# Kernel optimization log

Hardware: AMD Instinct MI355X
Metric: run time of the kernel (lower is better)

The kernel has to match this reference:

```python
import jax, jax.numpy as jnp
import numpy as np

NH = 4
MAX_BUF = 1024
EPS = 1e-5


def _ln(x, w, b):
    mu = jnp.mean(x, axis=-1, keepdims=True)
    var = jnp.var(x, axis=-1, keepdims=True)
    return (x - mu) * jax.lax.rsqrt(var + EPS) * w + b


def _mha(xq, xkv, w_qkv, b_qkv, w_o, b_o, key_mask=None):
    D = xq.shape[-1]
    dh = D // NH
    q = xq @ w_qkv[:D].T + b_qkv[:D]
    k = xkv @ w_qkv[D:2 * D].T + b_qkv[D:2 * D]
    v = xkv @ w_qkv[2 * D:].T + b_qkv[2 * D:]
    sp = lambda t: t.reshape(t.shape[0], t.shape[1], NH, dh).transpose(0, 2, 1, 3)
    q, k, v = sp(q), sp(k), sp(v)
    s = jnp.einsum('bhqd,bhkd->bhqk', q, k) / jnp.sqrt(jnp.asarray(dh, q.dtype))
    if key_mask is not None:
        s = jnp.where(key_mask[:, None, None, :], -1e9, s)
    a = jax.nn.softmax(s, axis=-1)
    o = jnp.einsum('bhqk,bhkd->bhqd', a, v)
    o = o.transpose(0, 2, 1, 3).reshape(o.shape[0], o.shape[2], D)
    return o @ w_o.T + b_o


def _conv1d(x, w, b):  # x: (B,C,T), w: (O,I,K) k=3 pad=1
    y = jax.lax.conv_general_dilated(x, w, (1,), [(1, 1)], dimension_numbers=('NCH', 'OIH', 'NCH'))
    return y + b[None, :, None]


def _vpred(xt, c1w, c1b, l1w, l1b, c2w, c2b, l2w, l2b, lw, lb):
    # Faithful to the torch module: LayerNorm(256)/Linear(256,1) act on the LAST
    # axis of the (B,256,T) conv output, which requires T == 256.
    h = _ln(jax.nn.relu(_conv1d(xt, c1w, c1b)), l1w, l1b)
    h = _ln(jax.nn.relu(_conv1d(h, c2w, c2b)), l2w, l2b)
    return (h @ lw.T + lb)[..., 0]  # (B, 256)


def _length_regulate(x, duration, lengths):
    # x: (B,T,D), duration: (B,T) float. Faithful parallel version of the
    # sequential scatter: tokens that are padded, have dur<=0, or would
    # overflow max_len are skipped (pos does not advance).
    B, T, D = x.shape
    durs = jnp.round(duration).astype(jnp.int32)
    max_len = jnp.clip(jnp.round(jnp.sum(duration, axis=1)).max().astype(jnp.int32), 0, MAX_BUF)
    valid_t = jnp.arange(T)[None, :] < lengths[:, None]

    def per_seq(dur_b, val_b):
        def step(pos, dv):
            d, v = dv
            ok = v & (d > 0) & (pos + d <= max_len)
            de = jnp.where(ok, d, 0)
            return pos + de, de
        return jax.lax.scan(step, jnp.asarray(0, jnp.int32), (dur_b, val_b))[1]

    dur_eff = jax.vmap(per_seq)(durs, valid_t)          # (B,T)
    ends = jnp.cumsum(dur_eff, axis=1)                  # token t fills [ends[t-1], ends[t])
    frames = jnp.arange(MAX_BUF)
    tok = jax.vmap(lambda e: jnp.searchsorted(e, frames, side='right'))(ends)  # (B,MAX_BUF)
    in_range = frames[None, :] < ends[:, -1:]
    g = jnp.take_along_axis(x, jnp.clip(tok, 0, T - 1)[..., None], axis=1)
    return jnp.where(in_range[..., None], g, jnp.zeros((), x.dtype))


def _forward(te, lengths, enc_qkv_w, enc_qkv_b, enc_out_w, enc_out_b, enc_ln1_w, enc_ln1_b, enc_ff1_w, enc_ff1_b, enc_ff2_w, enc_ff2_b, enc_ln2_w, enc_ln2_b, vp_c1_w, vp_c1_b, vp_l1_w, vp_l1_b, vp_c2_w, vp_c2_b, vp_l2_w, vp_l2_b, vp_lin_w, vp_lin_b, dec_sa_qkv_w, dec_sa_qkv_b, dec_sa_out_w, dec_sa_out_b, dec_ca_qkv_w, dec_ca_qkv_b, dec_ca_out_w, dec_ca_out_b, dec_ln1_w, dec_ln1_b, dec_ln2_w, dec_ln2_b, dec_ln3_w, dec_ln3_b, dec_ff1_w, dec_ff1_b, dec_ff2_w, dec_ff2_b, mel_w, mel_b):
    B, T, D = te.shape
    mask = jnp.arange(T)[None, :] >= lengths[:, None]  # src_key_padding_mask
    x = te
    for i in range(enc_qkv_w.shape[0]):  # post-norm TransformerEncoderLayer, gelu
        sa = _mha(x, x, enc_qkv_w[i], enc_qkv_b[i], enc_out_w[i], enc_out_b[i], mask)
        x = _ln(x + sa, enc_ln1_w[i], enc_ln1_b[i])
        ff = jax.nn.gelu(x @ enc_ff1_w[i].T + enc_ff1_b[i], approximate=False) @ enc_ff2_w[i].T + enc_ff2_b[i]
        x = _ln(x + ff, enc_ln2_w[i], enc_ln2_b[i])
    enc = x
    xt = enc.transpose(0, 2, 1)  # (B, D, T)
    duration, pitch, energy = [
        _vpred(xt, vp_c1_w[j], vp_c1_b[j], vp_l1_w[j], vp_l1_b[j], vp_c2_w[j], vp_c2_b[j], vp_l2_w[j], vp_l2_b[j], vp_lin_w[j], vp_lin_b[j])
        for j in range(3)]
    y = _length_regulate(enc, duration, lengths)  # (B, MAX_BUF, D)
    for i in range(dec_sa_qkv_w.shape[0]):  # post-norm TransformerDecoderLayer
        sa = _mha(y, y, dec_sa_qkv_w[i], dec_sa_qkv_b[i], dec_sa_out_w[i], dec_sa_out_b[i])
        y = _ln(y + sa, dec_ln1_w[i], dec_ln1_b[i])
        ca = _mha(y, enc, dec_ca_qkv_w[i], dec_ca_qkv_b[i], dec_ca_out_w[i], dec_ca_out_b[i])
        y = _ln(y + ca, dec_ln2_w[i], dec_ln2_b[i])
        ff = jax.nn.gelu(y @ dec_ff1_w[i].T + dec_ff1_b[i], approximate=False) @ dec_ff2_w[i].T + dec_ff2_b[i]
        y = _ln(y + ff, dec_ln3_w[i], dec_ln3_b[i])
    mel = (y @ mel_w.T + mel_b).transpose(0, 2, 1)  # (B, n_mel, MAX_BUF)
    return mel, duration, pitch, energy


def setup_inputs() -> dict:
    B, T, D, FF, NM, L = 32, 256, 256, 1024, 80, 4
    ks = iter(jax.random.split(jax.random.key(0), 80))

    def w(scale, *shape):
        return (scale * jax.random.normal(next(ks), shape)).astype(jnp.float32)

    z = lambda *s: jnp.zeros(s, jnp.float32)
    o = lambda *s: jnp.ones(s, jnp.float32)
    inp = {}
    inp['text_embeddings'] = jax.random.normal(next(ks), (B, T, D), jnp.float32)
    inp['text_lengths'] = jax.random.randint(next(ks), (B,), 64, T + 1, dtype=jnp.int32)
    inp.update(
        enc_qkv_w=w(0.02, L, 3 * D, D), enc_qkv_b=z(L, 3 * D), enc_out_w=w(0.02, L, D, D), enc_out_b=z(L, D),
        enc_ln1_w=o(L, D), enc_ln1_b=z(L, D), enc_ff1_w=w(0.02, L, FF, D), enc_ff1_b=z(L, FF),
        enc_ff2_w=w(0.02, L, D, FF), enc_ff2_b=z(L, D), enc_ln2_w=o(L, D), enc_ln2_b=z(L, D),
        vp_c1_w=w(0.05, 3, 256, D, 3), vp_c1_b=z(3, 256), vp_l1_w=o(3, 256), vp_l1_b=z(3, 256),
        vp_c2_w=w(0.05, 3, 256, 256, 3), vp_c2_b=z(3, 256), vp_l2_w=o(3, 256), vp_l2_b=z(3, 256),
        vp_lin_w=w(0.1, 3, 1, 256), vp_lin_b=jnp.array([[4.0], [0.0], [0.0]], jnp.float32),
        dec_sa_qkv_w=w(0.02, L, 3 * D, D), dec_sa_qkv_b=z(L, 3 * D), dec_sa_out_w=w(0.02, L, D, D), dec_sa_out_b=z(L, D),
        dec_ca_qkv_w=w(0.02, L, 3 * D, D), dec_ca_qkv_b=z(L, 3 * D), dec_ca_out_w=w(0.02, L, D, D), dec_ca_out_b=z(L, D),
        dec_ln1_w=o(L, D), dec_ln1_b=z(L, D), dec_ln2_w=o(L, D), dec_ln2_b=z(L, D), dec_ln3_w=o(L, D), dec_ln3_b=z(L, D),
        dec_ff1_w=w(0.02, L, FF, D), dec_ff1_b=z(L, FF), dec_ff2_w=w(0.02, L, D, FF), dec_ff2_b=z(L, D),
        mel_w=w(0.02, NM, D), mel_b=z(NM))
    return inp


def reference(text_embeddings, text_lengths, enc_qkv_w, enc_qkv_b, enc_out_w, enc_out_b, enc_ln1_w, enc_ln1_b, enc_ff1_w, enc_ff1_b, enc_ff2_w, enc_ff2_b, enc_ln2_w, enc_ln2_b, vp_c1_w, vp_c1_b, vp_l1_w, vp_l1_b, vp_c2_w, vp_c2_b, vp_l2_w, vp_l2_b, vp_lin_w, vp_lin_b, dec_sa_qkv_w, dec_sa_qkv_b, dec_sa_out_w, dec_sa_out_b, dec_ca_qkv_w, dec_ca_qkv_b, dec_ca_out_w, dec_ca_out_b, dec_ln1_w, dec_ln1_b, dec_ln2_w, dec_ln2_b, dec_ln3_w, dec_ln3_b, dec_ff1_w, dec_ff1_b, dec_ff2_w, dec_ff2_b, mel_w, mel_b):
    return _forward(text_embeddings, text_lengths, enc_qkv_w, enc_qkv_b, enc_out_w, enc_out_b, enc_ln1_w, enc_ln1_b, enc_ff1_w, enc_ff1_b, enc_ff2_w, enc_ff2_b, enc_ln2_w, enc_ln2_b, vp_c1_w, vp_c1_b, vp_l1_w, vp_l1_b, vp_c2_w, vp_c2_b, vp_l2_w, vp_l2_b, vp_lin_w, vp_lin_b, dec_sa_qkv_w, dec_sa_qkv_b, dec_sa_out_w, dec_sa_out_b, dec_ca_qkv_w, dec_ca_qkv_b, dec_ca_out_w, dec_ca_out_b, dec_ln1_w, dec_ln1_b, dec_ln2_w, dec_ln2_b, dec_ln3_w, dec_ln3_b, dec_ff1_w, dec_ff1_b, dec_ff2_w, dec_ff2_b, mel_w, mel_b)
```

## Files before the change

kernel.cpp:

```cpp
#include <hip/hip_runtime.h>
#include <hip/hip_bf16.h>
#include <cstdint>
#include <cstddef>


#define B_ 32
#define T_ 256
#define D_ 256
#define NH_ 4
#define FF_ 1024
#define MAXBUF_ 1024
#define NMEL_ 80

typedef __attribute__((ext_vector_type(8))) short short8;
typedef __attribute__((ext_vector_type(4))) float f32x4;

__device__ __forceinline__ unsigned short f2bf(float x) {
  unsigned int u = __float_as_uint(x);
  return (unsigned short)((u + 0x7fffu + ((u >> 16) & 1u)) >> 16);
}
__device__ __forceinline__ float bf2f(unsigned short h) {
  return __uint_as_float(((unsigned int)h) << 16);
}

#define GLD16(g, s)                                                         \
  __builtin_amdgcn_global_load_lds(                                         \
      (__attribute__((address_space(1))) void*)(g),                         \
      (__attribute__((address_space(3))) void*)(s), 16, 0, 0)

__global__ __launch_bounds__(256) void gemm_k(
    const float* __restrict__ A, const float* __restrict__ W,
    const float* __restrict__ bias, float* __restrict__ C,
    int M, int N, int K, int epi)
{
  __shared__ float As[16][64];
  __shared__ float Ws[16][64];
  const int tid = threadIdx.x;
  const int tx = tid & 15, ty = tid >> 4;
  const int bm = blockIdx.x * 64, bn = blockIdx.y * 64;
  const int lm = tid & 63, lk = tid >> 6;
  float acc[4][4] = {{0.f,0.f,0.f,0.f},{0.f,0.f,0.f,0.f},{0.f,0.f,0.f,0.f},{0.f,0.f,0.f,0.f}};
  const bool aok = (bm + lm) < M;
  const bool wok = (bn + lm) < N;
  const float* Ap = A + (size_t)(bm + lm) * K + lk * 4;
  const float* Wp = W + (size_t)(bn + lm) * K + lk * 4;
  for (int k0 = 0; k0 < K; k0 += 16) {
    float4 av = make_float4(0.f, 0.f, 0.f, 0.f);
    float4 wv = make_float4(0.f, 0.f, 0.f, 0.f);
    if (aok) av = *(const float4*)(Ap + k0);
    if (wok) wv = *(const float4*)(Wp + k0);
    As[lk*4+0][lm] = av.x; As[lk*4+1][lm] = av.y; As[lk*4+2][lm] = av.z; As[lk*4+3][lm] = av.w;
    Ws[lk*4+0][lm] = wv.x; Ws[lk*4+1][lm] = wv.y; Ws[lk*4+2][lm] = wv.z; Ws[lk*4+3][lm] = wv.w;
    __syncthreads();
#pragma unroll
    for (int kk = 0; kk < 16; ++kk) {
      float4 a4 = *(const float4*)&As[kk][ty * 4];
      float4 b4 = *(const float4*)&Ws[kk][tx * 4];
      float aa[4] = {a4.x, a4.y, a4.z, a4.w};
      float bb[4] = {b4.x, b4.y, b4.z, b4.w};
#pragma unroll
      for (int i = 0; i < 4; ++i)
#pragma unroll
        for (int j = 0; j < 4; ++j)
          acc[i][j] += aa[i] * bb[j];
    }
    __syncthreads();
  }
#pragma unroll
  for (int i = 0; i < 4; ++i) {
    int gm = bm + ty * 4 + i;
    if (gm >= M) continue;
#pragma unroll
    for (int j = 0; j < 4; ++j) {
      int gn = bn + tx * 4 + j;
      if (gn >= N) continue;
      float v = acc[i][j] + bias[gn];
      if (epi == 1) v = 0.5f * v * (1.0f + erff(v * 0.70710678118654752f));
      C[(size_t)gm * N + gn] = v;
    }
  }
}

__global__ __launch_bounds__(256, 2) void gemm2_k(
    const float* __restrict__ A, const float* __restrict__ W,
    const float* __restrict__ bias, float* __restrict__ C,
    int M, int N, int K, int epi)
{
  __shared__ float As[16][128];
  __shared__ float Bs[16][128];
  const int tid = threadIdx.x;
  const int tx = tid & 15, ty = tid >> 4;
  const int bm = blockIdx.x * 128, bn = blockIdx.y * 128;
  const int r = tid & 127, ks = (tid >> 7) * 8;
  f32x4 acc[8][2];
#pragma unroll
  for (int i = 0; i < 8; ++i) {
    acc[i][0] = (f32x4){0.f, 0.f, 0.f, 0.f};
    acc[i][1] = (f32x4){0.f, 0.f, 0.f, 0.f};
  }
  const float* Ap = A + (size_t)(bm + r) * K + ks;
  const float* Wp = W + (size_t)(bn + r) * K + ks;
  for (int k0 = 0; k0 < K; k0 += 16) {
    float4 a0 = *(const float4*)(Ap + k0);
    float4 a1 = *(const float4*)(Ap + k0 + 4);
    float4 w0 = *(const float4*)(Wp + k0);
    float4 w1 = *(const float4*)(Wp + k0 + 4);
    __syncthreads();
    As[ks+0][r] = a0.x; As[ks+1][r] = a0.y; As[ks+2][r] = a0.z; As[ks+3][r] = a0.w;
    As[ks+4][r] = a1.x; As[ks+5][r] = a1.y; As[ks+6][r] = a1.z; As[ks+7][r] = a1.w;
    Bs[ks+0][r] = w0.x; Bs[ks+1][r] = w0.y; Bs[ks+2][r] = w0.z; Bs[ks+3][r] = w0.w;
    Bs[ks+4][r] = w1.x; Bs[ks+5][r] = w1.y; Bs[ks+6][r] = w1.z; Bs[ks+7][r] = w1.w;
    __syncthreads();
#pragma unroll
    for (int kk = 0; kk < 16; ++kk) {
      f32x4 bA = *(const f32x4*)&Bs[kk][tx * 4];
      f32x4 bB = *(const f32x4*)&Bs[kk][tx * 4 + 64];
      float4 aA = *(const float4*)&As[kk][ty * 4];
      float4 aB = *(const float4*)&As[kk][ty * 4 + 64];
      float av[8] = {aA.x, aA.y, aA.z, aA.w, aB.x, aB.y, aB.z, aB.w};
#pragma unroll
      for (int i = 0; i < 8; ++i) {
        acc[i][0] += bA * av[i];
        acc[i][1] += bB * av[i];
      }
    }
  }
#pragma unroll
  for (int i = 0; i < 8; ++i) {
    int gm = bm + (i >> 2) * 64 + ty * 4 + (i & 3);
#pragma unroll
    for (int half = 0; half < 2; ++half) {
      int gn = bn + half * 64 + tx * 4;
      float4 o;
      o.x = acc[i][half][0] + bias[gn + 0];
      o.y = acc[i][half][1] + bias[gn + 1];
      o.z = acc[i][half][2] + bias[gn + 2];
      o.w = acc[i][half][3] + bias[gn + 3];
      if (epi == 1) {
        o.x = 0.5f * o.x * (1.0f + erff(o.x * 0.70710678118654752f));
        o.y = 0.5f * o.y * (1.0f + erff(o.y * 0.70710678118654752f));
        o.z = 0.5f * o.z * (1.0f + erff(o.z * 0.70710678118654752f));
        o.w = 0.5f * o.w * (1.0f + erff(o.w * 0.70710678118654752f));
      }
      *(float4*)(C + (size_t)gm * N + gn) = o;
    }
  }
}

__global__ __launch_bounds__(256) void attn_k(
    const float* __restrict__ Qp, int qStride,
    const float* __restrict__ Kp, int kStride,
    const float* __restrict__ Vp, int vStride,
    float* __restrict__ Op, int Tq, int Tkv,
    const int* __restrict__ lengths)
{
  const int b = blockIdx.z, h = blockIdx.y, qt = blockIdx.x;
  const int tid = threadIdx.x;
  const int tx = tid & 15, ty = tid >> 4;
  const int lr = tid & 63, lq = tid >> 6;

  __shared__ float Qs[64][64];
  __shared__ float KT[64][64];
  __shared__ float Sm[64][65];

  {
    const float* q = Qp + (size_t)(b * Tq + qt * 64 + lr) * qStride + h * 64 + lq * 16;
    float4 v0 = ((const float4*)q)[0];
    float4 v1 = ((const float4*)q)[1];
    float4 v2 = ((const float4*)q)[2];
    float4 v3 = ((const float4*)q)[3];
    *(float4*)&Qs[lr][lq*16 + 0]  = v0;
    *(float4*)&Qs[lr][lq*16 + 4]  = v1;
    *(float4*)&Qs[lr][lq*16 + 8]  = v2;
    *(float4*)&Qs[lr][lq*16 + 12] = v3;
  }

  float m_reg[4], l_reg[4], o[4][4];
#pragma unroll
  for (int i = 0; i < 4; ++i) {
    m_reg[i] = -INFINITY; l_reg[i] = 0.f;
#pragma unroll
    for (int j = 0; j < 4; ++j) o[i][j] = 0.f;
  }

  const int len_b = lengths ? lengths[b] : 0x7fffffff;
  const int nkt = Tkv >> 6;

  for (int kt = 0; kt < nkt; ++kt) {
    __syncthreads();
    {
      const float* kp = Kp + (size_t)(b * Tkv + kt * 64 + lr) * kStride + h * 64 + lq * 16;
      float4 v[4];
      v[0] = ((const float4*)kp)[0]; v[1] = ((const float4*)kp)[1];
      v[2] = ((const float4*)kp)[2]; v[3] = ((const float4*)kp)[3];
#pragma unroll
      for (int u = 0; u < 4; ++u) {
        KT[lq*16 + u*4 + 0][lr] = v[u].x;
        KT[lq*16 + u*4 + 1][lr] = v[u].y;
        KT[lq*16 + u*4 + 2][lr] = v[u].z;
        KT[lq*16 + u*4 + 3][lr] = v[u].w;
      }
    }
    __syncthreads();

    float s[4][4] = {{0.f,0.f,0.f,0.f},{0.f,0.f,0.f,0.f},{0.f,0.f,0.f,0.f},{0.f,0.f,0.f,0.f}};
#pragma unroll
    for (int d4 = 0; d4 < 16; ++d4) {
      float4 qv[4], kv[4];
#pragma unroll
      for (int i = 0; i < 4; ++i) qv[i] = *(const float4*)&Qs[ty*4 + i][d4*4];
#pragma unroll
      for (int dd = 0; dd < 4; ++dd) kv[dd] = *(const float4*)&KT[d4*4 + dd][tx*4];
#pragma unroll
      for (int i = 0; i < 4; ++i) {
        s[i][0] += qv[i].x*kv[0].x + qv[i].y*kv[1].x + qv[i].z*kv[2].x + qv[i].w*kv[3].x;
        s[i][1] += qv[i].x*kv[0].y + qv[i].y*kv[1].y + qv[i].z*kv[2].y + qv[i].w*kv[3].y;
        s[i][2] += qv[i].x*kv[0].z + qv[i].y*kv[1].z + qv[i].z*kv[2].z + qv[i].w*kv[3].z;
        s[i][3] += qv[i].x*kv[0].w + qv[i].y*kv[1].w + qv[i].z*kv[2].w + qv[i].w*kv[3].w;
      }
    }

    float alpha[4];
#pragma unroll
    for (int i = 0; i < 4; ++i) {
      float pm = -INFINITY;
#pragma unroll
      for (int j = 0; j < 4; ++j) {
        int kg = kt * 64 + tx * 4 + j;
        float v = s[i][j] * 0.125f;
        if (kg >= len_b) v = -1e9f;
        s[i][j] = v;
        pm = fmaxf(pm, v);
      }
#pragma unroll
      for (int off = 1; off < 16; off <<= 1) pm = fmaxf(pm, __shfl_xor(pm, off));
      float mn = fmaxf(m_reg[i], pm);
      alpha[i] = expf(m_reg[i] - mn);
      float ls = 0.f;
#pragma unroll
      for (int j = 0; j < 4; ++j) {
        float p = expf(s[i][j] - mn);
        Sm[ty*4 + i][tx*4 + j] = p;
        ls += p;
      }
#pragma unroll
      for (int off = 1; off < 16; off <<= 1) ls += __shfl_xor(ls, off);
      l_reg[i] = l_reg[i] * alpha[i] + ls;
      m_reg[i] = mn;
    }
    __syncthreads();

    {
      const float* vp = Vp + (size_t)(b * Tkv + kt * 64 + lr) * vStride + h * 64 + lq * 16;
      float4 v0 = ((const float4*)vp)[0];
      float4 v1 = ((const float4*)vp)[1];
      float4 v2 = ((const float4*)vp)[2];
      float4 v3 = ((const float4*)vp)[3];
      *(float4*)&KT[lr][lq*16 + 0]  = v0;
      *(float4*)&KT[lr][lq*16 + 4]  = v1;
      *(float4*)&KT[lr][lq*16 + 8]  = v2;
      *(float4*)&KT[lr][lq*16 + 12] = v3;
    }
    __syncthreads();

#pragma unroll
    for (int i = 0; i < 4; ++i) {
      o[i][0] *= alpha[i]; o[i][1] *= alpha[i]; o[i][2] *= alpha[i]; o[i][3] *= alpha[i];
    }
#pragma unroll 8
    for (int c = 0; c < 64; ++c) {
      float4 vv = *(const float4*)&KT[c][tx * 4];
#pragma unroll
      for (int i = 0; i < 4; ++i) {
        float p = Sm[ty*4 + i][c];
        o[i][0] += p * vv.x; o[i][1] += p * vv.y; o[i][2] += p * vv.z; o[i][3] += p * vv.w;
      }
    }
  }

#pragma unroll
  for (int i = 0; i < 4; ++i) {
    float inv = 1.f / l_reg[i];
    float4 r;
    r.x = o[i][0] * inv; r.y = o[i][1] * inv; r.z = o[i][2] * inv; r.w = o[i][3] * inv;
    *(float4*)(Op + (size_t)(b * Tq + qt * 64 + ty * 4 + i) * 256 + h * 64 + tx * 4) = r;
  }
}

__global__ __launch_bounds__(256) void gemm_bf_k(
    const unsigned short* __restrict__ A, const unsigned short* __restrict__ W,
    const float* __restrict__ bias, unsigned short* __restrict__ C,
    int M, int N, int K, int epi)
{
  __shared__ __align__(16) short As[128 * 32];
  __shared__ __align__(16) short Bs[128 * 32];
  const int tid = threadIdx.x;
  const int lane = tid & 63, w = tid >> 6;
  const int g = lane >> 4, li = lane & 15;
  const int wr = (w >> 1) * 64, wc = (w & 1) * 64;
  const int bm = blockIdx.x * 128, bn = blockIdx.y * 128;

  f32x4 acc[4][4];
#pragma unroll
  for (int m = 0; m < 4; ++m)
#pragma unroll
    for (int n = 0; n < 4; ++n)
      acc[m][n] = (f32x4){0.f, 0.f, 0.f, 0.f};

  const int srow = tid >> 2, scol = (tid & 3) * 8;
  const unsigned short* Ag = A + (size_t)(bm + srow) * K + scol;
  const unsigned short* Wg = W + (size_t)(bn + srow) * K + scol;

  for (int k0 = 0; k0 < K; k0 += 32) {
    __syncthreads();
    GLD16(Ag + k0, &As[tid * 8]);
    GLD16(Ag + k0 + (size_t)64 * K, &As[tid * 8 + 2048]);
    GLD16(Wg + k0, &Bs[tid * 8]);
    GLD16(Wg + k0 + (size_t)64 * K, &Bs[tid * 8 + 2048]);
    __syncthreads();
    short8 af[4], bf[4];
#pragma unroll
    for (int m = 0; m < 4; ++m) af[m] = *(const short8*)&As[(wr + m * 16 + li) * 32 + g * 8];
#pragma unroll
    for (int n = 0; n < 4; ++n) bf[n] = *(const short8*)&Bs[(wc + n * 16 + li) * 32 + g * 8];
#pragma unroll
    for (int m = 0; m < 4; ++m)
#pragma unroll
      for (int n = 0; n < 4; ++n)
        acc[m][n] = __builtin_amdgcn_mfma_f32_16x16x32_bf16(af[m], bf[n], acc[m][n], 0, 0, 0);
  }

#pragma unroll
  for (int m = 0; m < 4; ++m) {
#pragma unroll
    for (int n = 0; n < 4; ++n) {
      int col = bn + wc + n * 16 + li;
      float bv = bias[col];
#pragma unroll
      for (int r = 0; r < 4; ++r) {
        int row = bm + wr + m * 16 + g * 4 + r;
        float v = acc[m][n][r] + bv;
        if (epi == 1) v = 0.5f * v * (1.0f + erff(v * 0.70710678118654752f));
        C[(size_t)row * N + col] = f2bf(v);
      }
    }
  }
}

__global__ __launch_bounds__(256) void attn_bf_k(
    const unsigned short* __restrict__ Qp, int qStride,
    const unsigned short* __restrict__ Kp, int kStride,
    const unsigned short* __restrict__ Vp, int vStride,
    unsigned short* __restrict__ Op, int Tq, int Tkv)
{
  int b, h, qt;
  {
    const int nqt = gridDim.x, nh = gridDim.y, nbh = gridDim.y * gridDim.z;
    if ((nbh & 7) == 0) {
      int linear = blockIdx.x + nqt * (blockIdx.y + gridDim.y * blockIdx.z);
      int xcd = linear & 7, idx = linear >> 3;
      int bh = xcd * (nbh >> 3) + idx / nqt;
      qt = idx - (idx / nqt) * nqt;
      h = bh % nh; b = bh / nh;
    } else { qt = blockIdx.x; h = blockIdx.y; b = blockIdx.z; }
  }
  const int tid = threadIdx.x;
  const int lane = tid & 63, w = tid >> 6;
  const int g = lane >> 4, li = lane & 15;

  __shared__ __align__(16) short Qs[64 * 64];
  __shared__ __align__(16) short Ks[64 * 64];
  __shared__ __align__(16) short VT[64 * 64];
  __shared__ __align__(16) short Ps[64 * 64];

  {
    const int r0 = tid >> 3, seg = tid & 7;
#pragma unroll
    for (int i = 0; i < 2; ++i) {
      int r = r0 + i * 32;
      short8 v = *(const short8*)(Qp + (size_t)(b * Tq + qt * 64 + r) * qStride + h * 64 + seg * 8);
      *(short8*)&Qs[r * 64 + ((seg ^ (r & 7)) << 3)] = v;
    }
  }
  __syncthreads();

  short8 aq[2];
#pragma unroll
  for (int ks = 0; ks < 2; ++ks) {
    int row = w * 16 + li;
    aq[ks] = *(const short8*)&Qs[row * 64 + (((ks * 4 + g) ^ (row & 7)) << 3)];
  }

  float m_reg[4], l_reg[4];
  f32x4 o[4];
#pragma unroll
  for (int r = 0; r < 4; ++r) { m_reg[r] = -INFINITY; l_reg[r] = 0.f; }
#pragma unroll
  for (int n = 0; n < 4; ++n) o[n] = (f32x4){0.f, 0.f, 0.f, 0.f};

  const int nkt = Tkv >> 6;
  for (int kt = 0; kt < nkt; ++kt) {
    __syncthreads();
    {
      const int r0 = tid >> 3, seg = tid & 7;
#pragma unroll
      for (int i = 0; i < 2; ++i) {
        int r = r0 + i * 32;
        short8 kv = *(const short8*)(Kp + (size_t)(b * Tkv + kt * 64 + r) * kStride + h * 64 + seg * 8);
        *(short8*)&Ks[r * 64 + ((seg ^ (r & 7)) << 3)] = kv;
      }
    }
    {
      const int rv = tid & 63, wv_ = tid >> 6;
#pragma unroll
      for (int i = 0; i < 2; ++i) {
        int seg = wv_ * 2 + i;
        short8 vv = *(const short8*)(Vp + (size_t)(b * Tkv + kt * 64 + rv) * vStride + h * 64 + seg * 8);
#pragma unroll
        for (int j = 0; j < 8; ++j) {
          int d = seg * 8 + j;
          VT[d * 64 + (rv ^ ((d & 7) << 3))] = vv[j];
        }
      }
    }
    __syncthreads();

    f32x4 s[4];
#pragma unroll
    for (int n = 0; n < 4; ++n) {
      f32x4 acc = (f32x4){0.f, 0.f, 0.f, 0.f};
#pragma unroll
      for (int ks = 0; ks < 2; ++ks) {
        int key = n * 16 + li;
        short8 bk = *(const short8*)&Ks[key * 64 + (((ks * 4 + g) ^ (key & 7)) << 3)];
        acc = __builtin_amdgcn_mfma_f32_16x16x32_bf16(aq[ks], bk, acc, 0, 0, 0);
      }
      s[n] = acc * 0.125f;
    }

    float alpha[4];
#pragma unroll
    for (int r = 0; r < 4; ++r) {
      float pm = fmaxf(fmaxf(s[0][r], s[1][r]), fmaxf(s[2][r], s[3][r]));
#pragma unroll
      for (int off = 1; off < 16; off <<= 1) pm = fmaxf(pm, __shfl_xor(pm, off));
      float mn = fmaxf(m_reg[r], pm);
      alpha[r] = expf(m_reg[r] - mn);
      float ls = 0.f;
      int row = w * 16 + g * 4 + r;
#pragma unroll
      for (int n = 0; n < 4; ++n) {
        float p = expf(s[n][r] - mn);
        ls += p;
        int col = n * 16 + li;
        Ps[row * 64 + (col ^ ((row & 7) << 3))] = (short)f2bf(p);
      }
#pragma unroll
      for (int off = 1; off < 16; off <<= 1) ls += __shfl_xor(ls, off);
      l_reg[r] = l_reg[r] * alpha[r] + ls;
      m_reg[r] = mn;
    }

    f32x4 al = (f32x4){alpha[0], alpha[1], alpha[2], alpha[3]};
#pragma unroll
    for (int n = 0; n < 4; ++n) o[n] *= al;
    short8 ap[2];
#pragma unroll
    for (int ks = 0; ks < 2; ++ks) {
      int row = w * 16 + li;
      ap[ks] = *(const short8*)&Ps[row * 64 + (((ks * 4 + g) ^ (row & 7)) << 3)];
    }
#pragma unroll
    for (int n = 0; n < 4; ++n) {
#pragma unroll
      for (int ks = 0; ks < 2; ++ks) {
        int d = n * 16 + li;
        short8 bv = *(const short8*)&VT[d * 64 + (((ks * 4 + g) ^ (d & 7)) << 3)];
        o[n] = __builtin_amdgcn_mfma_f32_16x16x32_bf16(ap[ks], bv, o[n], 0, 0, 0);
      }
    }
  }

#pragma unroll
  for (int n = 0; n < 4; ++n) {
#pragma unroll
    for (int r = 0; r < 4; ++r) {
      float v = o[n][r] / l_reg[r];
      Op[(size_t)(b * Tq + qt * 64 + w * 16 + g * 4 + r) * 256 + h * 64 + n * 16 + li] = f2bf(v);
    }
  }
}

__global__ __launch_bounds__(256) void addln_k(
    const float* __restrict__ X, const float* __restrict__ R,
    const float* __restrict__ w, const float* __restrict__ bias,
    float* __restrict__ Out, int rows)
{
  int tid = threadIdx.x, wv = tid >> 6, ln = tid & 63;
  int row = blockIdx.x * 4 + wv;
  if (row >= rows) return;
  const float* xp = X + (size_t)row * 256;
  float v[4];
#pragma unroll
  for (int u = 0; u < 4; ++u) v[u] = xp[u * 64 + ln];
  if (R) {
    const float* rp = R + (size_t)row * 256;
#pragma unroll
    for (int u = 0; u < 4; ++u) v[u] += rp[u * 64 + ln];
  }
  float s = v[0] + v[1] + v[2] + v[3];
#pragma unroll
  for (int off = 1; off < 64; off <<= 1) s += __shfl_xor(s, off);
  float mean = s * (1.f / 256.f);
  float c[4], sq = 0.f;
#pragma unroll
  for (int u = 0; u < 4; ++u) { c[u] = v[u] - mean; sq += c[u] * c[u]; }
#pragma unroll
  for (int off = 1; off < 64; off <<= 1) sq += __shfl_xor(sq, off);
  float rs = 1.f / sqrtf(sq * (1.f / 256.f) + 1e-5f);
  float* op = Out + (size_t)row * 256;
#pragma unroll
  for (int u = 0; u < 4; ++u)
    op[u * 64 + ln] = c[u] * rs * w[u * 64 + ln] + bias[u * 64 + ln];
}

__global__ __launch_bounds__(256) void addln2_k(
    const float* __restrict__ X, const unsigned short* __restrict__ Rbf,
    const float* __restrict__ w, const float* __restrict__ bias,
    float* __restrict__ Out, unsigned short* __restrict__ OutBf, int rows)
{
  int tid = threadIdx.x, wv = tid >> 6, ln = tid & 63;
  int row = blockIdx.x * 4 + wv;
  if (row >= rows) return;
  const float* xp = X + (size_t)row * 256;
  const unsigned short* rp = Rbf + (size_t)row * 256;
  float v[4];
#pragma unroll
  for (int u = 0; u < 4; ++u) v[u] = xp[u * 64 + ln] + bf2f(rp[u * 64 + ln]);
  float s = v[0] + v[1] + v[2] + v[3];
#pragma unroll
  for (int off = 1; off < 64; off <<= 1) s += __shfl_xor(s, off);
  float mean = s * (1.f / 256.f);
  float c[4], sq = 0.f;
#pragma unroll
  for (int u = 0; u < 4; ++u) { c[u] = v[u] - mean; sq += c[u] * c[u]; }
#pragma unroll
  for (int off = 1; off < 64; off <<= 1) sq += __shfl_xor(sq, off);
  float rs = 1.f / sqrtf(sq * (1.f / 256.f) + 1e-5f);
  float* op = Out + (size_t)row * 256;
  unsigned short* ob = OutBf + (size_t)row * 256;
#pragma unroll
  for (int u = 0; u < 4; ++u) {
    float y = c[u] * rs * w[u * 64 + ln] + bias[u * 64 + ln];
    op[u * 64 + ln] = y;
    ob[u * 64 + ln] = f2bf(y);
  }
}

__global__ void cvt_k(const float* __restrict__ in, unsigned short* __restrict__ out, int n)
{
  int i = (blockIdx.x * 256 + threadIdx.x) * 4;
  if (i >= n) return;
  float4 v = *(const float4*)(in + i);
  unsigned short o[4] = {f2bf(v.x), f2bf(v.y), f2bf(v.z), f2bf(v.w)};
  *(ushort4*)(out + i) = *(ushort4*)o;
}

__global__ __launch_bounds__(256) void conv_k(
    const float* __restrict__ X, const float* __restrict__ Wt,
    const float* __restrict__ bias, float* __restrict__ Yo, int relu)
{
  const int b = blockIdx.z;
  const int o0 = blockIdx.y * 64, t0 = blockIdx.x * 64;
  const int tid = threadIdx.x, tx = tid & 15, ty = tid >> 4;
  __shared__ float xs[16][66];
  __shared__ float ws_s[64][48];
  float acc[4][4] = {{0.f,0.f,0.f,0.f},{0.f,0.f,0.f,0.f},{0.f,0.f,0.f,0.f},{0.f,0.f,0.f,0.f}};
  for (int i0 = 0; i0 < 256; i0 += 16) {
    for (int idx = tid; idx < 16 * 66; idx += 256) {
      int ic = idx / 66, tt = idx - ic * 66;
      int t = t0 + tt - 1;
      xs[ic][tt] = (t >= 0 && t < 256) ? X[((size_t)b * 256 + (i0 + ic)) * 256 + t] : 0.f;
    }
    for (int f4 = tid; f4 < 768; f4 += 256) {
      int oo = f4 / 12, seg = f4 - oo * 12;
      float4 v = *(const float4*)(Wt + (size_t)(o0 + oo) * 768 + i0 * 3 + seg * 4);
      *(float4*)&ws_s[oo][seg * 4] = v;
    }
    __syncthreads();
#pragma unroll
    for (int ic = 0; ic < 16; ++ic) {
      float xr[6];
#pragma unroll
      for (int u = 0; u < 6; ++u) xr[u] = xs[ic][tx * 4 + u];
#pragma unroll
      for (int i = 0; i < 4; ++i) {
        const float* wr = &ws_s[ty * 4 + i][ic * 3];
        float w0 = wr[0], w1 = wr[1], w2 = wr[2];
#pragma unroll
        for (int j = 0; j < 4; ++j)
          acc[i][j] += w0 * xr[j] + w1 * xr[j + 1] + w2 * xr[j + 2];
      }
    }
    __syncthreads();
  }
#pragma unroll
  for (int i = 0; i < 4; ++i) {
    int oo = o0 + ty * 4 + i;
    float bv = bias[oo];
#pragma unroll
    for (int j = 0; j < 4; ++j) {
      float v = acc[i][j] + bv;
      if (relu) v = fmaxf(v, 0.f);
      Yo[((size_t)b * 256 + oo) * 256 + t0 + tx * 4 + j] = v;
    }
  }
}

__global__ void transp_k(const float* __restrict__ In, float* __restrict__ Out)
{
  int b = blockIdx.z, t0 = blockIdx.x * 32, d0 = blockIdx.y * 32;
  __shared__ float tile[32][33];
  int tx = threadIdx.x, ty = threadIdx.y;
#pragma unroll
  for (int q = 0; q < 4; ++q)
    tile[ty + q * 8][tx] = In[((size_t)b * 256 + t0 + ty + q * 8) * 256 + d0 + tx];
  __syncthreads();
#pragma unroll
  for (int q = 0; q < 4; ++q)
    Out[((size_t)b * 256 + d0 + ty + q * 8) * 256 + t0 + tx] = tile[tx][ty + q * 8];
}

__global__ __launch_bounds__(256) void rowdot_k(
    const float* __restrict__ H, const float* __restrict__ lw,
    const float* __restrict__ lb, float* __restrict__ of32,
    float* __restrict__ oout, int rows)
{
  int tid = threadIdx.x, wv = tid >> 6, ln = tid & 63;
  int row = blockIdx.x * 4 + wv;
  if (row >= rows) return;
  const float* hp = H + (size_t)row * 256;
  float s = 0.f;
#pragma unroll
  for (int u = 0; u < 4; ++u) s += hp[u * 64 + ln] * lw[u * 64 + ln];
#pragma unroll
  for (int off = 1; off < 64; off <<= 1) s += __shfl_xor(s, off);
  if (ln == 0) {
    float v = s + lb[0];
    of32[row] = v;
    oout[row] = v;
  }
}

__global__ void maxlen_k(const float* __restrict__ dur, int* __restrict__ ml)
{
  __shared__ float rnds[32];
  int tid = threadIdx.x, wv = tid >> 6, ln = tid & 63;
  for (int b = wv; b < 32; b += 4) {
    const float* dp = dur + (size_t)b * 256;
    float s = dp[ln] + dp[64 + ln] + dp[128 + ln] + dp[192 + ln];
#pragma unroll
    for (int off = 1; off < 64; off <<= 1) s += __shfl_xor(s, off);
    if (ln == 0) rnds[b] = rintf(s);
  }
  __syncthreads();
  if (tid == 0) {
    float m = rnds[0];
    for (int b = 1; b < 32; ++b) m = fmaxf(m, rnds[b]);
    int v = (int)m;
    v = v < 0 ? 0 : (v > MAXBUF_ ? MAXBUF_ : v);
    *ml = v;
  }
}

__global__ void reg_k(const float* __restrict__ dur, const int* __restrict__ lens,
                      const int* __restrict__ ml, int* __restrict__ tok)
{
  int b = blockIdx.x;
  __shared__ float sdur[256];
  __shared__ int ends[256];
  int tid = threadIdx.x;
  sdur[tid] = dur[(size_t)b * 256 + tid];
  __syncthreads();
  if (tid == 0) {
    int maxlen = *ml, len = lens[b], pos = 0;
    for (int t = 0; t < 256; ++t) {
      int d = (int)rintf(sdur[t]);
      bool ok = (t < len) && (d > 0) && (pos + d <= maxlen);
      if (ok) pos += d;
      ends[t] = pos;
    }
  }
  __syncthreads();
  int total = ends[255];
  for (int f = tid; f < MAXBUF_; f += 256) {
    int lo = 0, hi = 256;
    while (lo < hi) { int mid = (lo + hi) >> 1; if (ends[mid] <= f) lo = mid + 1; else hi = mid; }
    int tc = lo > 255 ? 255 : lo;
    tok[(size_t)b * MAXBUF_ + f] = (f < total) ? tc : -1;
  }
}

__global__ void gather_k(const float* __restrict__ enc, const int* __restrict__ tok,
                         float* __restrict__ Y)
{
  int rf = blockIdx.x;
  int b = rf >> 10;
  int t = tok[rf];
  float4* dst = (float4*)(Y + (size_t)rf * 256);
  int ln = threadIdx.x;
  if (t >= 0) {
    const float4* src = (const float4*)(enc + ((size_t)b * 256 + t) * 256);
    dst[ln] = src[ln];
  } else {
    dst[ln] = make_float4(0.f, 0.f, 0.f, 0.f);
  }
}

__global__ __launch_bounds__(256) void meltr_k(
    const float* __restrict__ MEL, float* __restrict__ out)
{
  int b = blockIdx.z, m0 = blockIdx.y * 16, f0 = blockIdx.x * 64;
  __shared__ float t[16][65];
  int tid = threadIdx.x;
  {
    int f_i = tid >> 4, m_i = tid & 15;
#pragma unroll
    for (int q = 0; q < 4; ++q)
      t[m_i][f_i + q * 16] = MEL[((size_t)b * 1024 + f0 + f_i + q * 16) * 80 + m0 + m_i];
  }
  __syncthreads();
  {
    int f = tid & 63, my = tid >> 6;
#pragma unroll
    for (int q = 0; q < 4; ++q) {
      int m = my * 4 + q;
      out[((size_t)b * NMEL_ + m0 + m) * MAXBUF_ + f0 + f] = t[m][f];
    }
  }
}

extern "C" void kernel_launch(void* const* d_in, const int* in_sizes, int n_in,
                              void* d_out, int out_size, void* d_ws, size_t ws_size,
                              hipStream_t stream)
{
  (void)in_sizes; (void)n_in; (void)out_size;

  const float* te   = (const float*)d_in[0];
  const int*   lens = (const int*)d_in[1];
  const float* e_qkv_w = (const float*)d_in[2];
  const float* e_qkv_b = (const float*)d_in[3];
  const float* e_out_w = (const float*)d_in[4];
  const float* e_out_b = (const float*)d_in[5];
  const float* e_ln1_w = (const float*)d_in[6];
  const float* e_ln1_b = (const float*)d_in[7];
  const float* e_ff1_w = (const float*)d_in[8];
  const float* e_ff1_b = (const float*)d_in[9];
  const float* e_ff2_w = (const float*)d_in[10];
  const float* e_ff2_b = (const float*)d_in[11];
  const float* e_ln2_w = (const float*)d_in[12];
  const float* e_ln2_b = (const float*)d_in[13];
  const float* c1w = (const float*)d_in[14];
  const float* c1b = (const float*)d_in[15];
  const float* l1w = (const float*)d_in[16];
  const float* l1b = (const float*)d_in[17];
  const float* c2w = (const float*)d_in[18];
  const float* c2b = (const float*)d_in[19];
  const float* l2w = (const float*)d_in[20];
  const float* l2b = (const float*)d_in[21];
  const float* linw = (const float*)d_in[22];
  const float* linb = (const float*)d_in[23];
  const float* d_sa_qkv_w = (const float*)d_in[24];
  const float* d_sa_qkv_b = (const float*)d_in[25];
  const float* d_sa_out_w = (const float*)d_in[26];
  const float* d_sa_out_b = (const float*)d_in[27];
  const float* d_ca_qkv_w = (const float*)d_in[28];
  const float* d_ca_qkv_b = (const float*)d_in[29];
  const float* d_ca_out_w = (const float*)d_in[30];
  const float* d_ca_out_b = (const float*)d_in[31];
  const float* d_ln1_w = (const float*)d_in[32];
  const float* d_ln1_b = (const float*)d_in[33];
  const float* d_ln2_w = (const float*)d_in[34];
  const float* d_ln2_b = (const float*)d_in[35];
  const float* d_ln3_w = (const float*)d_in[36];
  const float* d_ln3_b = (const float*)d_in[37];
  const float* d_ff1_w = (const float*)d_in[38];
  const float* d_ff1_b = (const float*)d_in[39];
  const float* d_ff2_w = (const float*)d_in[40];
  const float* d_ff2_b = (const float*)d_in[41];
  const float* melw = (const float*)d_in[42];
  const float* melb = (const float*)d_in[43];
  float* out = (float*)d_out;

  char* p = (char*)d_ws;
  float* Y   = (float*)p;            p += 8388608ull * 4;
  float* ENC = (float*)p;            p += 2097152ull * 4;
  unsigned short* ENCbf = (unsigned short*)p; p += 2097152ull * 2;
  unsigned short* Wsaqkv = (unsigned short*)p; p += 786432ull * 2;
  unsigned short* Wsaout = (unsigned short*)p; p += 262144ull * 2;
  unsigned short* Wcaqkv = (unsigned short*)p; p += 786432ull * 2;
  unsigned short* Wcaout = (unsigned short*)p; p += 262144ull * 2;
  unsigned short* Wff1   = (unsigned short*)p; p += 1048576ull * 2;
  unsigned short* Wff2   = (unsigned short*)p; p += 1048576ull * 2;
  float* DUR = (float*)p;            p += 24576ull * 4;
  int* TOK   = (int*)p;              p += 32768ull * 4;
  int* MAXL  = (int*)p;              p += 4096;
  size_t fixed_b = (size_t)(p - (char*)d_ws);

  int grp = 1;
  {
    const int cand[6] = {32, 16, 8, 4, 2, 1};
    for (int c = 0; c < 6; ++c) {
      if (fixed_b + (size_t)cand[c] * 1835008ull * 2 <= ws_size) { grp = cand[c]; break; }
    }
  }
  unsigned short* REG = (unsigned short*)p;
  unsigned short* Ybf   = REG;
  unsigned short* ADDbf = REG + (size_t)grp * 262144;
  unsigned short* AObf  = REG + (size_t)grp * 524288;
  unsigned short* UN    = REG + (size_t)grp * 786432;
  int grp_e = grp * 2 > 32 ? 32 : grp * 2;
  float* P0e = (float*)REG;
  float* P1e = P0e + (size_t)grp_e * 262144;
  float* P2e = P1e + (size_t)grp_e * 65536;
  float* ENCT = Y;
  float* H1   = Y + 2097152;
  float* H2   = Y + 4194304;
  float* MEL  = ENC;

  auto gemm = [&](const float* A, const float* W, const float* bias, float* C,
                  int M, int N, int K, int epi) {
    dim3 g((M + 63) / 64, (N + 63) / 64);
    gemm_k<<<g, dim3(256), 0, stream>>>(A, W, bias, C, M, N, K, epi);
  };
  auto gemm2 = [&](const float* A, const float* W, const float* bias, float* C,
                   int M, int N, int K, int epi) {
    dim3 g(M / 128, N / 128);
    gemm2_k<<<g, dim3(256), 0, stream>>>(A, W, bias, C, M, N, K, epi);
  };
  auto gemm_bf = [&](const unsigned short* A, const unsigned short* W, const float* bias,
                     unsigned short* C, int M, int N, int K, int epi) {
    dim3 g(M / 128, N / 128);
    gemm_bf_k<<<g, dim3(256), 0, stream>>>(A, W, bias, C, M, N, K, epi);
  };
  auto addln = [&](const float* X, const float* R, const float* w, const float* b,
                   float* O, int rows) {
    addln_k<<<dim3((rows + 3) / 4), dim3(256), 0, stream>>>(X, R, w, b, O, rows);
  };
  auto addln2 = [&](const float* X, const unsigned short* Rbf, const float* w, const float* b,
                    float* O, unsigned short* Obf, int rows) {
    addln2_k<<<dim3((rows + 3) / 4), dim3(256), 0, stream>>>(X, Rbf, w, b, O, Obf, rows);
  };
  auto cvt = [&](const float* in, unsigned short* o, int n) {
    cvt_k<<<dim3(n / 1024), dim3(256), 0, stream>>>(in, o, n);
  };

  cvt(d_sa_qkv_w, Wsaqkv, 786432);
  cvt(d_sa_out_w, Wsaout, 262144);
  cvt(d_ca_qkv_w, Wcaqkv, 786432);
  cvt(d_ca_out_w, Wcaout, 262144);
  cvt(d_ff1_w, Wff1, 1048576);
  cvt(d_ff2_w, Wff2, 1048576);

  for (int i = 0; i < 4; ++i) {
    for (int g0 = 0; g0 < B_; g0 += grp_e) {
      int rows = grp_e * T_;
      const size_t off = (size_t)g0 * T_ * D_;
      const float* xin = (i == 0) ? te + off : ENC + off;
      gemm2(xin, e_qkv_w + (size_t)i * 196608, e_qkv_b + i * 768, P0e, rows, 768, 256, 0);
      attn_k<<<dim3(T_ / 64, NH_, grp_e), dim3(256), 0, stream>>>(
          P0e, 768, P0e + 256, 768, P0e + 512, 768, P1e, T_, T_, lens + g0);
      gemm2(P1e, e_out_w + (size_t)i * 65536, e_out_b + i * 256, P2e, rows, 256, 256, 0);
      addln(xin, P2e, e_ln1_w + i * 256, e_ln1_b + i * 256, ENC + off, rows);
      gemm2(ENC + off, e_ff1_w + (size_t)i * 262144, e_ff1_b + i * 1024, P0e, rows, 1024, 256, 1);
      gemm2(P0e, e_ff2_w + (size_t)i * 262144, e_ff2_b + i * 256, P2e, rows, 256, 1024, 0);
      addln(ENC + off, P2e, e_ln2_w + i * 256, e_ln2_b + i * 256, ENC + off, rows);
    }
  }
  cvt(ENC, ENCbf, 2097152);

  transp_k<<<dim3(8, 8, B_), dim3(32, 8), 0, stream>>>(ENC, ENCT);
  for (int j = 0; j < 3; ++j) {
    conv_k<<<dim3(4, 4, B_), dim3(256), 0, stream>>>(
        ENCT, c1w + (size_t)j * 196608, c1b + j * 256, H1, 1);
    addln(H1, nullptr, l1w + j * 256, l1b + j * 256, H1, B_ * T_);
    conv_k<<<dim3(4, 4, B_), dim3(256), 0, stream>>>(
        H1, c2w + (size_t)j * 196608, c2b + j * 256, H2, 1);
    addln(H2, nullptr, l2w + j * 256, l2b + j * 256, H2, B_ * T_);
    rowdot_k<<<dim3(B_ * T_ / 4), dim3(256), 0, stream>>>(
        H2, linw + j * 256, linb + j, DUR + (size_t)j * 8192,
        out + 2621440 + (size_t)j * 8192, B_ * T_);
  }

  maxlen_k<<<dim3(1), dim3(256), 0, stream>>>(DUR, MAXL);
  reg_k<<<dim3(B_), dim3(256), 0, stream>>>(DUR, lens, MAXL, TOK);
  gather_k<<<dim3(B_ * MAXBUF_), dim3(64), 0, stream>>>(ENC, TOK, Y);

  for (int i = 0; i < 4; ++i) {
    for (int g0 = 0; g0 < B_; g0 += grp) {
      int rows = grp * MAXBUF_;
      float* Yg = Y + (size_t)g0 * MAXBUF_ * D_;
      if (i == 0 || grp != B_)
        cvt(Yg, Ybf, rows * 256);
      gemm_bf(Ybf, Wsaqkv + (size_t)i * 196608, d_sa_qkv_b + i * 768, UN, rows, 768, 256, 0);
      attn_bf_k<<<dim3(MAXBUF_ / 64, NH_, grp), dim3(256), 0, stream>>>(
          UN, 768, UN + 256, 768, UN + 512, 768, AObf, MAXBUF_, MAXBUF_);
      gemm_bf(AObf, Wsaout + (size_t)i * 65536, d_sa_out_b + i * 256, ADDbf, rows, 256, 256, 0);
      addln2(Yg, ADDbf, d_ln1_w + i * 256, d_ln1_b + i * 256, Yg, Ybf, rows);
      gemm_bf(Ybf, Wcaqkv + (size_t)i * 196608, d_ca_qkv_b + i * 768, UN, rows, 256, 256, 0);
      gemm_bf(ENCbf + (size_t)g0 * 65536, Wcaqkv + (size_t)i * 196608 + 65536,
              d_ca_qkv_b + i * 768 + 256, UN + (size_t)grp * 262144, grp * T_, 512, 256, 0);
      attn_bf_k<<<dim3(MAXBUF_ / 64, NH_, grp), dim3(256), 0, stream>>>(
          UN, 256, UN + (size_t)grp * 262144, 512, UN + (size_t)grp * 262144 + 256, 512,
          AObf, MAXBUF_, T_);
      gemm_bf(AObf, Wcaout + (size_t)i * 65536, d_ca_out_b + i * 256, ADDbf, rows, 256, 256, 0);
      addln2(Yg, ADDbf, d_ln2_w + i * 256, d_ln2_b + i * 256, Yg, Ybf, rows);
      gemm_bf(Ybf, Wff1 + (size_t)i * 262144, d_ff1_b + i * 1024, UN, rows, 1024, 256, 1);
      gemm_bf(UN, Wff2 + (size_t)i * 262144, d_ff2_b + i * 256, ADDbf, rows, 256, 1024, 0);
      addln2(Yg, ADDbf, d_ln3_w + i * 256, d_ln3_b + i * 256, Yg, Ybf, rows);
    }
  }

  gemm(Y, melw, melb, MEL, B_ * MAXBUF_, NMEL_, 256, 0);
  meltr_k<<<dim3(16, 5, B_), dim3(256), 0, stream>>>(MEL, out);
}
```

Measured before the change: 3.571 ms.

## Pre-transpose V in separate kernel and double query tile per attention block

Adds a kernel that writes V transposed to global memory once per head and key tile. The attention kernel can then load V^T with vector loads instead of scattered per-element shared-memory stores. The attention block now handles 128 query rows, so each K/V tile is reused by twice as many queries. It also adds MFMA priority hints and fast __expf. In exchange there is an extra launch and extra global traffic for VT, more shared memory and registers, and a launch-bounds occupancy hint.

```diff
diff --git a/kernel.cpp b/kernel.cpp
--- a/kernel.cpp
+++ b/kernel.cpp
@@ -347,10 +347,36 @@
   }
 }
 
-__global__ __launch_bounds__(256) void attn_bf_k(
+__global__ __launch_bounds__(256) void trv_k(
+    const unsigned short* __restrict__ V, int vStride,
+    unsigned short* __restrict__ VT, int Tkv)
+{
+  const int kt = blockIdx.x, h = blockIdx.y, b = blockIdx.z;
+  __shared__ short t[64][65];
+  const int tid = threadIdx.x;
+  const int r0 = tid >> 3, seg = tid & 7;
+#pragma unroll
+  for (int i = 0; i < 2; ++i) {
+    int r = r0 + i * 32;
+    short8 v = *(const short8*)(V + (size_t)(b * Tkv + kt * 64 + r) * vStride + h * 64 + seg * 8);
+    *(short8*)&t[r][seg * 8] = v;
+  }
+  __syncthreads();
+#pragma unroll
+  for (int i = 0; i < 2; ++i) {
+    int d = r0 + i * 32;
+    int k0 = seg * 8;
+    short o[8];
+#pragma unroll
+    for (int j = 0; j < 8; ++j) o[j] = t[k0 + j][d];
+    *(short8*)(VT + ((size_t)(b * NH_ + h) * 64 + d) * Tkv + kt * 64 + k0) = *(short8*)o;
+  }
+}
+
+__global__ __launch_bounds__(256, 2) void attn_bf_k(
     const unsigned short* __restrict__ Qp, int qStride,
     const unsigned short* __restrict__ Kp, int kStride,
-    const unsigned short* __restrict__ Vp, int vStride,
+    const unsigned short* __restrict__ VTg,
     unsigned short* __restrict__ Op, int Tq, int Tkv)
 {
   int b, h, qt;
@@ -368,37 +394,44 @@
   const int lane = tid & 63, w = tid >> 6;
   const int g = lane >> 4, li = lane & 15;
 
-  __shared__ __align__(16) short Qs[64 * 64];
+  __shared__ __align__(16) short Qs[128 * 64];
   __shared__ __align__(16) short Ks[64 * 64];
-  __shared__ __align__(16) short VT[64 * 64];
-  __shared__ __align__(16) short Ps[64 * 64];
+  __shared__ __align__(16) short VTs[64 * 64];
+  __shared__ __align__(16) short Ps[128 * 64];
 
   {
     const int r0 = tid >> 3, seg = tid & 7;
 #pragma unroll
-    for (int i = 0; i < 2; ++i) {
+    for (int i = 0; i < 4; ++i) {
       int r = r0 + i * 32;
-      short8 v = *(const short8*)(Qp + (size_t)(b * Tq + qt * 64 + r) * qStride + h * 64 + seg * 8);
+      short8 v = *(const short8*)(Qp + (size_t)(b * Tq + qt * 128 + r) * qStride + h * 64 + seg * 8);
       *(short8*)&Qs[r * 64 + ((seg ^ (r & 7)) << 3)] = v;
     }
   }
   __syncthreads();
 
-  short8 aq[2];
-#pragma unroll
-  for (int ks = 0; ks < 2; ++ks) {
-    int row = w * 16 + li;
-    aq[ks] = *(const short8*)&Qs[row * 64 + (((ks * 4 + g) ^ (row & 7)) << 3)];
-  }
-
-  float m_reg[4], l_reg[4];
-  f32x4 o[4];
-#pragma unroll
-  for (int r = 0; r < 4; ++r) { m_reg[r] = -INFINITY; l_reg[r] = 0.f; }
-#pragma unroll
-  for (int n = 0; n < 4; ++n) o[n] = (f32x4){0.f, 0.f, 0.f, 0.f};
+  short8 aq[2][2];
+#pragma unroll
+  for (int m = 0; m < 2; ++m)
+#pragma unroll
+    for (int ks = 0; ks < 2; ++ks) {
+      int row = w * 32 + m * 16 + li;
+      aq[m][ks] = *(const short8*)&Qs[row * 64 + (((ks * 4 + g) ^ (row & 7)) << 3)];
+    }
+
+  float m_reg[2][4], l_reg[2][4];
+  f32x4 o[2][4];
+#pragma unroll
+  for (int m = 0; m < 2; ++m)
+#pragma unroll
+    for (int r = 0; r < 4; ++r) { m_reg[m][r] = -INFINITY; l_reg[m][r] = 0.f; }
+#pragma unroll
+  for (int m = 0; m < 2; ++m)
+#pragma unroll
+    for (int n = 0; n < 4; ++n) o[m][n] = (f32x4){0.f, 0.f, 0.f, 0.f};
 
   const int nkt = Tkv >> 6;
+  const unsigned short* vt = VTg + (size_t)(b * NH_ + h) * 64 * Tkv;
   for (int kt = 0; kt < nkt; ++kt) {
     __syncthreads();
     {
@@ -408,87 +441,91 @@
         int r = r0 + i * 32;
         short8 kv = *(const short8*)(Kp + (size_t)(b * Tkv + kt * 64 + r) * kStride + h * 64 + seg * 8);
         *(short8*)&Ks[r * 64 + ((seg ^ (r & 7)) << 3)] = kv;
-      }
-    }
-    {
-      const int rv = tid & 63, wv_ = tid >> 6;
-#pragma unroll
-      for (int i = 0; i < 2; ++i) {
-        int seg = wv_ * 2 + i;
-        short8 vv = *(const short8*)(Vp + (size_t)(b * Tkv + kt * 64 + rv) * vStride + h * 64 + seg * 8);
-#pragma unroll
-        for (int j = 0; j < 8; ++j) {
-          int d = seg * 8 + j;
-          VT[d * 64 + (rv ^ ((d & 7) << 3))] = vv[j];
+        short8 vv = *(const short8*)(vt + (size_t)r * Tkv + kt * 64 + seg * 8);
+        *(short8*)&VTs[r * 64 + ((seg ^ (r & 7)) << 3)] = vv;
+      }
+    }
+    __syncthreads();
+
+    f32x4 s[2][4];
+    __builtin_amdgcn_s_setprio(1);
+#pragma unroll
+    for (int m = 0; m < 2; ++m)
+#pragma unroll
+      for (int n = 0; n < 4; ++n) {
+        f32x4 acc = (f32x4){0.f, 0.f, 0.f, 0.f};
+#pragma unroll
+        for (int ks = 0; ks < 2; ++ks) {
+          int key = n * 16 + li;
+          short8 bk = *(const short8*)&Ks[key * 64 + (((ks * 4 + g) ^ (key & 7)) << 3)];
+          acc = __builtin_amdgcn_mfma_f32_16x16x32_bf16(aq[m][ks], bk, acc, 0, 0, 0);
         }
-      }
-    }
-    __syncthreads();
-
-    f32x4 s[4];
-#pragma unroll
-    for (int n = 0; n < 4; ++n) {
-      f32x4 acc = (f32x4){0.f, 0.f, 0.f, 0.f};
+        s[m][n] = acc * 0.125f;
+      }
+    __builtin_amdgcn_s_setprio(0);
+
+    float alpha[2][4];
+#pragma unroll
+    for (int m = 0; m < 2; ++m)
+#pragma unroll
+      for (int r = 0; r < 4; ++r) {
+        float pm = fmaxf(fmaxf(s[m][0][r], s[m][1][r]), fmaxf(s[m][2][r], s[m][3][r]));
+#pragma unroll
+        for (int off = 1; off < 16; off <<= 1) pm = fmaxf(pm, __shfl_xor(pm, off));
+        float mn = fmaxf(m_reg[m][r], pm);
+        alpha[m][r] = __expf(m_reg[m][r] - mn);
+        float ls = 0.f;
+        int row = w * 32 + m * 16 + g * 4 + r;
+#pragma unroll
+        for (int n = 0; n < 4; ++n) {
+          float p = __expf(s[m][n][r] - mn);
+          ls += p;
+          int col = n * 16 + li;
+          Ps[row * 64 + (col ^ ((row & 7) << 3))] = (short)f2bf(p);
+        }
+#pragma unroll
+        for (int off = 1; off < 16; off <<= 1) ls += __shfl_xor(ls, off);
+        l_reg[m][r] = l_reg[m][r] * alpha[m][r] + ls;
+        m_reg[m][r] = mn;
+      }
+
+#pragma unroll
+    for (int m = 0; m < 2; ++m) {
+      f32x4 al = (f32x4){alpha[m][0], alpha[m][1], alpha[m][2], alpha[m][3]};
+#pragma unroll
+      for (int n = 0; n < 4; ++n) o[m][n] *= al;
+    }
+    short8 ap[2][2];
+#pragma unroll
+    for (int m = 0; m < 2; ++m)
 #pragma unroll
       for (int ks = 0; ks < 2; ++ks) {
-        int key = n * 16 + li;
-        short8 bk = *(const short8*)&Ks[key * 64 + (((ks * 4 + g) ^ (key & 7)) << 3)];
-        acc = __builtin_amdgcn_mfma_f32_16x16x32_bf16(aq[ks], bk, acc, 0, 0, 0);
-      }
-      s[n] = acc * 0.125f;
-    }
-
-    float alpha[4];
-#pragma unroll
-    for (int r = 0; r < 4; ++r) {
-      float pm = fmaxf(fmaxf(s[0][r], s[1][r]), fmaxf(s[2][r], s[3][r]));
-#pragma unroll
-      for (int off = 1; off < 16; off <<= 1) pm = fmaxf(pm, __shfl_xor(pm, off));
-      float mn = fmaxf(m_reg[r], pm);
-      alpha[r] = expf(m_reg[r] - mn);
-      float ls = 0.f;
-      int row = w * 16 + g * 4 + r;
-#pragma unroll
-      for (int n = 0; n < 4; ++n) {
-        float p = expf(s[n][r] - mn);
-        ls += p;
-        int col = n * 16 + li;
-        Ps[row * 64 + (col ^ ((row & 7) << 3))] = (short)f2bf(p);
-      }
-#pragma unroll
-      for (int off = 1; off < 16; off <<= 1) ls += __shfl_xor(ls, off);
-      l_reg[r] = l_reg[r] * alpha[r] + ls;
-      m_reg[r] = mn;
-    }
-
-    f32x4 al = (f32x4){alpha[0], alpha[1], alpha[2], alpha[3]};
-#pragma unroll
-    for (int n = 0; n < 4; ++n) o[n] *= al;
-    short8 ap[2];
-#pragma unroll
-    for (int ks = 0; ks < 2; ++ks) {
-      int row = w * 16 + li;
-      ap[ks] = *(const short8*)&Ps[row * 64 + (((ks * 4 + g) ^ (row & 7)) << 3)];
-    }
-#pragma unroll
-    for (int n = 0; n < 4; ++n) {
-#pragma unroll
-      for (int ks = 0; ks < 2; ++ks) {
-        int d = n * 16 + li;
-        short8 bv = *(const short8*)&VT[d * 64 + (((ks * 4 + g) ^ (d & 7)) << 3)];
-        o[n] = __builtin_amdgcn_mfma_f32_16x16x32_bf16(ap[ks], bv, o[n], 0, 0, 0);
-      }
-    }
-  }
-
-#pragma unroll
-  for (int n = 0; n < 4; ++n) {
-#pragma unroll
-    for (int r = 0; r < 4; ++r) {
-      float v = o[n][r] / l_reg[r];
-      Op[(size_t)(b * Tq + qt * 64 + w * 16 + g * 4 + r) * 256 + h * 64 + n * 16 + li] = f2bf(v);
-    }
-  }
+        int row = w * 32 + m * 16 + li;
+        ap[m][ks] = *(const short8*)&Ps[row * 64 + (((ks * 4 + g) ^ (row & 7)) << 3)];
+      }
+    __builtin_amdgcn_s_setprio(1);
+#pragma unroll
+    for (int m = 0; m < 2; ++m)
+#pragma unroll
+      for (int n = 0; n < 4; ++n)
+#pragma unroll
+        for (int ks = 0; ks < 2; ++ks) {
+          int d = n * 16 + li;
+          short8 bv = *(const short8*)&VTs[d * 64 + (((ks * 4 + g) ^ (d & 7)) << 3)];
+          o[m][n] = __builtin_amdgcn_mfma_f32_16x16x32_bf16(ap[m][ks], bv, o[m][n], 0, 0, 0);
+        }
+    __builtin_amdgcn_s_setprio(0);
+  }
+
+#pragma unroll
+  for (int m = 0; m < 2; ++m)
+#pragma unroll
+    for (int n = 0; n < 4; ++n)
+#pragma unroll
+      for (int r = 0; r < 4; ++r) {
+        float v = o[m][n][r] / l_reg[m][r];
+        Op[(size_t)(b * Tq + qt * 128 + w * 32 + m * 16 + g * 4 + r) * 256 + h * 64 + n * 16 + li] = f2bf(v);
+      }
 }
 
 __global__ __launch_bounds__(256) void addln_k(
@@ -819,6 +856,7 @@
   unsigned short* ADDbf = REG + (size_t)grp * 262144;
   unsigned short* AObf  = REG + (size_t)grp * 524288;
   unsigned short* UN    = REG + (size_t)grp * 786432;
+  unsigned short* VTb   = REG + (size_t)grp * 1572864;
   int grp_e = grp * 2 > 32 ? 32 : grp * 2;
   float* P0e = (float*)REG;
   float* P1e = P0e + (size_t)grp_e * 262144;
@@ -903,16 +941,18 @@
       if (i == 0 || grp != B_)
         cvt(Yg, Ybf, rows * 256);
       gemm_bf(Ybf, Wsaqkv + (size_t)i * 196608, d_sa_qkv_b + i * 768, UN, rows, 768, 256, 0);
-      attn_bf_k<<<dim3(MAXBUF_ / 64, NH_, grp), dim3(256), 0, stream>>>(
-          UN, 768, UN + 256, 768, UN + 512, 768, AObf, MAXBUF_, MAXBUF_);
+      trv_k<<<dim3(MAXBUF_ / 64, NH_, grp), dim3(256), 0, stream>>>(UN + 512, 768, VTb, MAXBUF_);
+      attn_bf_k<<<dim3(MAXBUF_ / 128, NH_, grp), dim3(256), 0, stream>>>(
+          UN, 768, UN + 256, 768, VTb, AObf, MAXBUF_, MAXBUF_);
       gemm_bf(AObf, Wsaout + (size_t)i * 65536, d_sa_out_b + i * 256, ADDbf, rows, 256, 256, 0);
       addln2(Yg, ADDbf, d_ln1_w + i * 256, d_ln1_b + i * 256, Yg, Ybf, rows);
       gemm_bf(Ybf, Wcaqkv + (size_t)i * 196608, d_ca_qkv_b + i * 768, UN, rows, 256, 256, 0);
       gemm_bf(ENCbf + (size_t)g0 * 65536, Wcaqkv + (size_t)i * 196608 + 65536,
               d_ca_qkv_b + i * 768 + 256, UN + (size_t)grp * 262144, grp * T_, 512, 256, 0);
-      attn_bf_k<<<dim3(MAXBUF_ / 64, NH_, grp), dim3(256), 0, stream>>>(
-          UN, 256, UN + (size_t)grp * 262144, 512, UN + (size_t)grp * 262144 + 256, 512,
-          AObf, MAXBUF_, T_);
+      trv_k<<<dim3(T_ / 64, NH_, grp), dim3(256), 0, stream>>>(
+          UN + (size_t)grp * 262144 + 256, 512, VTb, T_);
+      attn_bf_k<<<dim3(MAXBUF_ / 128, NH_, grp), dim3(256), 0, stream>>>(
+          UN, 256, UN + (size_t)grp * 262144, 512, VTb, AObf, MAXBUF_, T_);
       gemm_bf(AObf, Wcaout + (size_t)i * 65536, d_ca_out_b + i * 256, ADDbf, rows, 256, 256, 0);
       addln2(Yg, ADDbf, d_ln2_w + i * 256, d_ln2_b + i * 256, Yg, Ybf, rows);
       gemm_bf(Ybf, Wff1 + (size_t)i * 262144, d_ff1_b + i * 1024, UN, rows, 1024, 256, 1);
```

After: 3.453 ms. 3.3% less time.
